# Optimization experiments

Measured on AMD Instinct MI355X. Metric: run time of the kernel, lower is better.

Reference implementation:

```python
import jax, jax.numpy as jnp
import numpy as np

DIM = 768
N_HEADS = 12
HEAD_DIM = DIM // N_HEADS
B, T = 2, 2048


def setup_inputs() -> dict:
    key = jax.random.key(0)
    ks = jax.random.split(key, 11)
    s = 0.02
    return {
        "q_in": jax.random.normal(ks[0], (B, T, DIM), jnp.float32),
        "k_in": jax.random.normal(ks[1], (B, T, DIM), jnp.float32),
        "v_in": jax.random.normal(ks[2], (B, T, DIM), jnp.float32),
        "Wq": jax.random.normal(ks[3], (DIM, DIM), jnp.float32) * s,
        "bq": jnp.zeros((DIM,), jnp.float32),
        "Wk": jax.random.normal(ks[4], (DIM, DIM), jnp.float32) * s,
        "bk": jnp.zeros((DIM,), jnp.float32),
        "Wv": jax.random.normal(ks[5], (DIM, DIM), jnp.float32) * s,
        "bv": jnp.zeros((DIM,), jnp.float32),
        "Wo": jax.random.normal(ks[6], (DIM, DIM), jnp.float32) * s,
        "bo": jnp.zeros((DIM,), jnp.float32),
    }


def reference(q_in, k_in, v_in, Wq, bq, Wk, bk, Wv, bv, Wo, bo):
    b, t, c = q_in.shape
    scale = HEAD_DIM ** -0.5
    # linear projections (torch Linear: x @ W.T + b)
    q = q_in @ Wq.T + bq
    k = k_in @ Wk.T + bk
    v = v_in @ Wv.T + bv
    # [b, t, h, d] -> [b, h, t, d]
    q = q.reshape(b, t, N_HEADS, HEAD_DIM).transpose(0, 2, 1, 3)
    k = k.reshape(b, t, N_HEADS, HEAD_DIM).transpose(0, 2, 1, 3)
    v = v.reshape(b, t, N_HEADS, HEAD_DIM).transpose(0, 2, 1, 3)
    scores = jnp.einsum("bhqd,bhkd->bhqk", q, k) * scale  # full TxT scores
    probs = jax.nn.softmax(scores, axis=-1)
    attn = jnp.einsum("bhqk,bhkd->bhqd", probs, v)
    attn = attn.transpose(0, 2, 1, 3).reshape(b, t, c)
    return attn @ Wo.T + bo
```

## Files before the change

kernel.cpp:

```cpp
#include <hip/hip_runtime.h>


typedef unsigned short u16;
typedef __attribute__((ext_vector_type(8))) short short8;
typedef __attribute__((ext_vector_type(4))) short short4v;
typedef __attribute__((ext_vector_type(4))) float float4v;

#define DIMC 768
#define NTOK 4096
#define NHD  12
#define HDD  64
#define SEQT 2048

#if __has_builtin(__builtin_amdgcn_mfma_f32_16x16x16bf16_1k)
#define HAVE_MFMA16 1
#else
#define HAVE_MFMA16 0
#endif

__device__ __forceinline__ u16 f2bf(float f) {
  union { float f; unsigned u; } v; v.f = f;
  unsigned r = v.u + 0x7fffu + ((v.u >> 16) & 1u);
  return (u16)(r >> 16);
}
__device__ __forceinline__ float bf2f(u16 u) {
  union { unsigned u; float f; } v; v.u = ((unsigned)u) << 16;
  return v.f;
}
__device__ __forceinline__ short4v u2s4(uint2 u) {
  union { uint2 u; short4v s; } v; v.u = u; return v.s;
}

__global__ __launch_bounds__(256) void cvt_all(
    const float* __restrict__ a0, const float* __restrict__ a1, const float* __restrict__ a2,
    const float* __restrict__ a3, const float* __restrict__ a4, const float* __restrict__ a5,
    const float* __restrict__ a6,
    u16* __restrict__ o0, u16* __restrict__ o1, u16* __restrict__ o2,
    u16* __restrict__ o3, u16* __restrict__ o4, u16* __restrict__ o5,
    u16* __restrict__ o6) {
  int bid = blockIdx.x;
  const float* s; u16* d; int inner;
  if (bid < 9216) {
    int z = bid / 3072; inner = bid - z * 3072;
    s = (z == 0) ? a0 : (z == 1) ? a1 : a2;
    d = (z == 0) ? o0 : (z == 1) ? o1 : o2;
  } else {
    int r = bid - 9216; int z = r / 576; inner = r - z * 576;
    s = (z == 0) ? a3 : (z == 1) ? a4 : (z == 2) ? a5 : a6;
    d = (z == 0) ? o3 : (z == 1) ? o4 : (z == 2) ? o5 : o6;
  }
  size_t i = ((size_t)inner * 256 + threadIdx.x) * 4;
  float4 v = *(const float4*)(s + i);
  *(ushort4*)(d + i) = make_ushort4(f2bf(v.x), f2bf(v.y), f2bf(v.z), f2bf(v.w));
}

__device__ __forceinline__ void gemm_mainloop3(
    const u16* __restrict__ X, const u16* __restrict__ W,
    int m0, int n0, u16* Als, u16* Bls, float4v acc[4][4]) {
  int tid = threadIdx.x;
  int sr = tid >> 3, sc = (tid & 7) * 8;
  int w = tid >> 6, lane = tid & 63, quad = lane >> 4, r15 = lane & 15;
  int wm = (w >> 1) * 64, wn = (w & 1) * 64;
  const u16* xp0 = X + (size_t)(m0 + sr) * DIMC + sc;
  const u16* xp1 = xp0 + 32 * DIMC;
  const u16* xp2 = xp0 + 64 * DIMC;
  const u16* xp3 = xp0 + 96 * DIMC;
  const u16* wp0 = W + (size_t)(n0 + sr) * DIMC + sc;
  const u16* wp1 = wp0 + 32 * DIMC;
  const u16* wp2 = wp0 + 64 * DIMC;
  const u16* wp3 = wp0 + 96 * DIMC;
  uint4 pa0 = *(const uint4*)xp0, pa1 = *(const uint4*)xp1;
  uint4 pa2 = *(const uint4*)xp2, pa3 = *(const uint4*)xp3;
  uint4 pb0 = *(const uint4*)wp0, pb1 = *(const uint4*)wp1;
  uint4 pb2 = *(const uint4*)wp2, pb3 = *(const uint4*)wp3;
  for (int k0 = 0; k0 < DIMC; k0 += 64) {
    __syncthreads();
    *(uint4*)(Als + sr * 72 + sc) = pa0;
    *(uint4*)(Als + (sr + 32) * 72 + sc) = pa1;
    *(uint4*)(Als + (sr + 64) * 72 + sc) = pa2;
    *(uint4*)(Als + (sr + 96) * 72 + sc) = pa3;
    *(uint4*)(Bls + sr * 72 + sc) = pb0;
    *(uint4*)(Bls + (sr + 32) * 72 + sc) = pb1;
    *(uint4*)(Bls + (sr + 64) * 72 + sc) = pb2;
    *(uint4*)(Bls + (sr + 96) * 72 + sc) = pb3;
    __syncthreads();
    int kn = k0 + 64;
    if (kn < DIMC) {
      pa0 = *(const uint4*)(xp0 + kn); pa1 = *(const uint4*)(xp1 + kn);
      pa2 = *(const uint4*)(xp2 + kn); pa3 = *(const uint4*)(xp3 + kn);
      pb0 = *(const uint4*)(wp0 + kn); pb1 = *(const uint4*)(wp1 + kn);
      pb2 = *(const uint4*)(wp2 + kn); pb3 = *(const uint4*)(wp3 + kn);
    }
    #pragma unroll
    for (int sk = 0; sk < 2; sk++) {
      short8 af[4], bf[4];
      #pragma unroll
      for (int mf = 0; mf < 4; mf++)
        af[mf] = *(const short8*)(Als + (wm + mf * 16 + r15) * 72 + sk * 32 + quad * 8);
      #pragma unroll
      for (int nf = 0; nf < 4; nf++)
        bf[nf] = *(const short8*)(Bls + (wn + nf * 16 + r15) * 72 + sk * 32 + quad * 8);
      #pragma unroll
      for (int mf = 0; mf < 4; mf++)
        #pragma unroll
        for (int nf = 0; nf < 4; nf++)
          acc[mf][nf] = __builtin_amdgcn_mfma_f32_16x16x32_bf16(af[mf], bf[nf], acc[mf][nf], 0, 0, 0);
    }
  }
}

__global__ __launch_bounds__(256, 2) void gemm_qkv(
    const u16* __restrict__ xq, const u16* __restrict__ xk, const u16* __restrict__ xv,
    const u16* __restrict__ wq, const u16* __restrict__ wk, const u16* __restrict__ wv,
    const float* __restrict__ bq, const float* __restrict__ bk, const float* __restrict__ bv,
    u16* __restrict__ Qh, u16* __restrict__ Kh, u16* __restrict__ Vt) {
  __shared__ __align__(16) u16 LS[2 * 128 * 72];
  u16* Als = LS;
  u16* Bls = LS + 128 * 72;
  int z = blockIdx.z;
  const u16* X = (z == 0) ? xq : (z == 1) ? xk : xv;
  const u16* W = (z == 0) ? wq : (z == 1) ? wk : wv;
  const float* bias = (z == 0) ? bq : (z == 1) ? bk : bv;
  int m0 = blockIdx.x * 128, n0 = blockIdx.y * 128;
  float4v acc[4][4];
  #pragma unroll
  for (int i = 0; i < 4; i++)
    #pragma unroll
    for (int j = 0; j < 4; j++)
      #pragma unroll
      for (int r = 0; r < 4; r++) acc[i][j][r] = 0.f;
  gemm_mainloop3(X, W, m0, n0, Als, Bls, acc);
  int tid = threadIdx.x, w = tid >> 6, lane = tid & 63, quad = lane >> 4, r15 = lane & 15;
  int wm = (w >> 1) * 64, wn = (w & 1) * 64;
  if (z == 2) {
    __syncthreads();
    u16* T = LS;
    #pragma unroll
    for (int mf = 0; mf < 4; mf++)
      #pragma unroll
      for (int nf = 0; nf < 4; nf++)
        #pragma unroll
        for (int rg = 0; rg < 4; rg++) {
          int mloc = wm + mf * 16 + quad * 4 + rg;
          int nloc = wn + nf * 16 + r15;
          T[nloc * 136 + mloc] = f2bf(acc[mf][nf][rg] + bias[n0 + nloc]);
        }
    __syncthreads();
    int r = tid >> 1, seg = tid & 1;
    int b = m0 >> 11, t0 = m0 & 2047;
    int h = (n0 + r) >> 6, d = (n0 + r) & 63;
    size_t base = (((size_t)(b * NHD + h)) * HDD + d) * SEQT + t0 + seg * 64;
    const u16* src = T + r * 136 + seg * 64;
    #pragma unroll
    for (int j = 0; j < 8; j++)
      *(uint4*)(Vt + base + j * 8) = *(const uint4*)(src + j * 8);
  } else {
    #pragma unroll
    for (int mf = 0; mf < 4; mf++)
      #pragma unroll
      for (int nf = 0; nf < 4; nf++)
        #pragma unroll
        for (int rg = 0; rg < 4; rg++) {
          int m = m0 + wm + mf * 16 + quad * 4 + rg;
          int n = n0 + wn + nf * 16 + r15;
          float val = acc[mf][nf][rg] + bias[n];
          if (z == 0) val *= 0.180336880f;
          int b = m >> 11, t = m & 2047, h = n >> 6, d = n & 63;
          u16 o = f2bf(val);
          size_t bh = (size_t)(b * NHD + h);
          if (z == 0) Qh[(bh * SEQT + t) * HDD + d] = o;
          else Kh[(bh * SEQT + t) * HDD + d] = o;
        }
  }
}

__global__ __launch_bounds__(256, 4) void attn_kernel(
    const u16* __restrict__ Qh, const u16* __restrict__ Kh, const u16* __restrict__ Vt,
    u16* __restrict__ Opart, float* __restrict__ Lpart) {
  __shared__ __align__(16) u16 Kls[64 * 64];
  __shared__ __align__(16) u16 Vls[64 * 64];
#if !HAVE_MFMA16
  __shared__ __align__(16) u16 Pls[4 * 32 * 64];
#endif
  int bh = blockIdx.y, sp = blockIdx.z, qt0 = blockIdx.x * 128;
  int tid = threadIdx.x, w = tid >> 6, lane = tid & 63, quad = lane >> 4, r15 = lane & 15;
  int qw = qt0 + w * 32;
  const int nt = 8;
  int kt0 = sp * (nt * 64);

  int rr = r15 & 7;
  int sx0 = (quad ^ rr) * 8;
  int sx1 = ((4 + quad) ^ rr) * 8;
  int q1 = quad >> 1, q0 = quad & 1;

  short8 qa[2][2];
  #pragma unroll
  for (int qs = 0; qs < 2; qs++) {
    const u16* qp = Qh + ((size_t)bh * SEQT + qw + qs * 16 + r15) * HDD + quad * 8;
    qa[qs][0] = *(const short8*)qp;
    qa[qs][1] = *(const short8*)(qp + 32);
  }
  float4v fzero;
  #pragma unroll
  for (int r = 0; r < 4; r++) fzero[r] = 0.f;

  float4v oacc[2][4];
  float lsum[2];
  #pragma unroll
  for (int qs = 0; qs < 2; qs++) {
    lsum[qs] = 0.f;
    #pragma unroll
    for (int dt = 0; dt < 4; dt++)
      #pragma unroll
      for (int r = 0; r < 4; r++) oacc[qs][dt][r] = 0.f;
  }

  const u16* Kbase = Kh + (size_t)bh * SEQT * HDD;
  const u16* Vbase = Vt + (size_t)bh * HDD * SEQT;
  int sr = tid >> 3, sc = (tid & 7) * 8;
  int sg = (((tid & 7) ^ (sr & 7)) * 8);

  uint4 pk0 = *(const uint4*)(Kbase + (size_t)(kt0 + sr) * HDD + sc);
  uint4 pk1 = *(const uint4*)(Kbase + (size_t)(kt0 + sr + 32) * HDD + sc);
  uint4 pv0 = *(const uint4*)(Vbase + (size_t)sr * SEQT + kt0 + sc);
  uint4 pv1 = *(const uint4*)(Vbase + (size_t)(sr + 32) * SEQT + kt0 + sc);

  for (int it = 0; it < nt; it++) {
    __syncthreads();
    *(uint4*)(Kls + sr * 64 + sg) = pk0;
    *(uint4*)(Kls + (sr + 32) * 64 + sg) = pk1;
    *(uint4*)(Vls + sr * 64 + sg) = pv0;
    *(uint4*)(Vls + (sr + 32) * 64 + sg) = pv1;
    __syncthreads();
    int nit = it + 1; if (nit == nt) nit = 0;
    int ktn = kt0 + nit * 64;
    pk0 = *(const uint4*)(Kbase + (size_t)(ktn + sr) * HDD + sc);
    pk1 = *(const uint4*)(Kbase + (size_t)(ktn + sr + 32) * HDD + sc);
    pv0 = *(const uint4*)(Vbase + (size_t)sr * SEQT + ktn + sc);
    pv1 = *(const uint4*)(Vbase + (size_t)(sr + 32) * SEQT + ktn + sc);

    __builtin_amdgcn_s_setprio(1);
#if HAVE_MFMA16
    #pragma unroll
    for (int nk = 0; nk < 4; nk++) {
      short8 k0 = *(const short8*)(Kls + (nk * 16 + r15) * 64 + sx0);
      short8 k1 = *(const short8*)(Kls + (nk * 16 + r15) * 64 + sx1);
      float4v z0 = __builtin_amdgcn_mfma_f32_16x16x32_bf16(k0, qa[0][0], fzero, 0, 0, 0);
      z0 = __builtin_amdgcn_mfma_f32_16x16x32_bf16(k1, qa[0][1], z0, 0, 0, 0);
      float4v z1 = __builtin_amdgcn_mfma_f32_16x16x32_bf16(k0, qa[1][0], fzero, 0, 0, 0);
      z1 = __builtin_amdgcn_mfma_f32_16x16x32_bf16(k1, qa[1][1], z1, 0, 0, 0);
      float a0 = __builtin_amdgcn_exp2f(z0[0]);
      float a1 = __builtin_amdgcn_exp2f(z0[1]);
      float a2 = __builtin_amdgcn_exp2f(z0[2]);
      float a3 = __builtin_amdgcn_exp2f(z0[3]);
      float b0 = __builtin_amdgcn_exp2f(z1[0]);
      float b1 = __builtin_amdgcn_exp2f(z1[1]);
      float b2 = __builtin_amdgcn_exp2f(z1[2]);
      float b3 = __builtin_amdgcn_exp2f(z1[3]);
      lsum[0] += (a0 + a1) + (a2 + a3);
      lsum[1] += (b0 + b1) + (b2 + b3);
      short4v pb0 = u2s4(make_uint2(
          __builtin_amdgcn_perm(__float_as_uint(a1), __float_as_uint(a0), 0x07060302u),
          __builtin_amdgcn_perm(__float_as_uint(a3), __float_as_uint(a2), 0x07060302u)));
      short4v pb1 = u2s4(make_uint2(
          __builtin_amdgcn_perm(__float_as_uint(b1), __float_as_uint(b0), 0x07060302u),
          __builtin_amdgcn_perm(__float_as_uint(b3), __float_as_uint(b2), 0x07060302u)));
      #pragma unroll
      for (int dt = 0; dt < 4; dt++) {
        uint2 vw = *(const uint2*)(Vls + (dt * 16 + r15) * 64 +
                                   (((nk * 2 + q1) ^ rr) * 8) + q0 * 4);
        short4v va = u2s4(vw);
        oacc[0][dt] = __builtin_amdgcn_mfma_f32_16x16x16bf16_1k(va, pb0, oacc[0][dt], 0, 0, 0);
        oacc[1][dt] = __builtin_amdgcn_mfma_f32_16x16x16bf16_1k(va, pb1, oacc[1][dt], 0, 0, 0);
      }
    }
#else
    u16* Pw = Pls + w * (32 * 64);
    #pragma unroll
    for (int nk = 0; nk < 4; nk++) {
      short8 k0 = *(const short8*)(Kls + (nk * 16 + r15) * 64 + sx0);
      short8 k1 = *(const short8*)(Kls + (nk * 16 + r15) * 64 + sx1);
      #pragma unroll
      for (int qs = 0; qs < 2; qs++) {
        float4v zv = __builtin_amdgcn_mfma_f32_16x16x32_bf16(k0, qa[qs][0], fzero, 0, 0, 0);
        zv = __builtin_amdgcn_mfma_f32_16x16x32_bf16(k1, qa[qs][1], zv, 0, 0, 0);
        float p0 = __builtin_amdgcn_exp2f(zv[0]);
        float p1 = __builtin_amdgcn_exp2f(zv[1]);
        float p2 = __builtin_amdgcn_exp2f(zv[2]);
        float p3 = __builtin_amdgcn_exp2f(zv[3]);
        lsum[qs] += (p0 + p1) + (p2 + p3);
        unsigned lo = __builtin_amdgcn_perm(__float_as_uint(p1), __float_as_uint(p0), 0x07060302u);
        unsigned hi = __builtin_amdgcn_perm(__float_as_uint(p3), __float_as_uint(p2), 0x07060302u);
        *(uint2*)(Pw + (qs * 16 + r15) * 64 + (((nk * 4 + quad) ^ (rr << 1)) << 2)) =
            make_uint2(lo, hi);
      }
    }
    short8 pa[2][2];
    #pragma unroll
    for (int qs = 0; qs < 2; qs++) {
      pa[qs][0] = *(const short8*)(Pw + (qs * 16 + r15) * 64 + sx0);
      pa[qs][1] = *(const short8*)(Pw + (qs * 16 + r15) * 64 + sx1);
    }
    #pragma unroll
    for (int dt = 0; dt < 4; dt++) {
      short8 v0 = *(const short8*)(Vls + (dt * 16 + r15) * 64 + sx0);
      short8 v1 = *(const short8*)(Vls + (dt * 16 + r15) * 64 + sx1);
      #pragma unroll
      for (int qs = 0; qs < 2; qs++) {
        oacc[qs][dt] = __builtin_amdgcn_mfma_f32_16x16x32_bf16(pa[qs][0], v0, oacc[qs][dt], 0, 0, 0);
        oacc[qs][dt] = __builtin_amdgcn_mfma_f32_16x16x32_bf16(pa[qs][1], v1, oacc[qs][dt], 0, 0, 0);
      }
    }
#endif
    __builtin_amdgcn_s_setprio(0);
  }
  size_t obase = ((size_t)sp * 2 * NHD + bh) * SEQT + qw;
#if HAVE_MFMA16
  #pragma unroll
  for (int qs = 0; qs < 2; qs++) {
    u16* orow = Opart + (obase + qs * 16 + r15) * HDD + quad * 4;
    #pragma unroll
    for (int dt = 0; dt < 4; dt++) {
      u16 c0 = f2bf(oacc[qs][dt][0]);
      u16 c1 = f2bf(oacc[qs][dt][1]);
      u16 c2 = f2bf(oacc[qs][dt][2]);
      u16 c3 = f2bf(oacc[qs][dt][3]);
      *(uint2*)(orow + dt * 16) =
          make_uint2((unsigned)c0 | ((unsigned)c1 << 16),
                     (unsigned)c2 | ((unsigned)c3 << 16));
    }
  }
#else
  #pragma unroll
  for (int qs = 0; qs < 2; qs++)
    #pragma unroll
    for (int rg = 0; rg < 4; rg++) {
      u16* orow = Opart + (obase + qs * 16 + quad * 4 + rg) * HDD;
      #pragma unroll
      for (int dt = 0; dt < 4; dt++) orow[dt * 16 + r15] = f2bf(oacc[qs][dt][rg]);
    }
#endif
  #pragma unroll
  for (int qs = 0; qs < 2; qs++) {
    float s = lsum[qs];
    s += __shfl_xor(s, 16, 64);
    s += __shfl_xor(s, 32, 64);
    if (quad == 0) Lpart[obase + qs * 16 + r15] = s;
  }
}

__global__ __launch_bounds__(256) void merge_kernel(
    const u16* __restrict__ Opart, const float* __restrict__ Lpart, u16* __restrict__ X2) {
  const size_t NXe = (size_t)2 * NHD * SEQT * HDD;
  const size_t LS = (size_t)2 * NHD * SEQT;
  int tid = threadIdx.x;
  int row = blockIdx.x * 32 + (tid >> 3);
  int dcol = (tid & 7) * 8;
  int bh = row >> 11, t = row & 2047;
  size_t off = (size_t)row * HDD + dcol;
  float inv = 1.0f / (Lpart[row] + Lpart[row + LS] +
                      Lpart[row + 2 * LS] + Lpart[row + 3 * LS]);
  int b = bh / NHD, h = bh % NHD;
  u16 o[8];
  #pragma unroll
  for (int half = 0; half < 2; half++) {
    ushort4 a = *(const ushort4*)(Opart + off + half * 4);
    ushort4 c = *(const ushort4*)(Opart + off + NXe + half * 4);
    ushort4 e = *(const ushort4*)(Opart + off + 2 * NXe + half * 4);
    ushort4 g = *(const ushort4*)(Opart + off + 3 * NXe + half * 4);
    o[half * 4 + 0] = f2bf((bf2f(a.x) + bf2f(c.x) + bf2f(e.x) + bf2f(g.x)) * inv);
    o[half * 4 + 1] = f2bf((bf2f(a.y) + bf2f(c.y) + bf2f(e.y) + bf2f(g.y)) * inv);
    o[half * 4 + 2] = f2bf((bf2f(a.z) + bf2f(c.z) + bf2f(e.z) + bf2f(g.z)) * inv);
    o[half * 4 + 3] = f2bf((bf2f(a.w) + bf2f(c.w) + bf2f(e.w) + bf2f(g.w)) * inv);
  }
  *(uint4*)(X2 + ((size_t)b * SEQT + t) * DIMC + h * HDD + dcol) = *(uint4*)o;
}

__global__ __launch_bounds__(256, 2) void gemm_out(
    const u16* __restrict__ X2, const u16* __restrict__ wo,
    const float* __restrict__ bo, float* __restrict__ out) {
  __shared__ __align__(16) u16 LS[2 * 128 * 72];
  u16* Als = LS;
  u16* Bls = LS + 128 * 72;
  int m0 = blockIdx.x * 128, n0 = blockIdx.y * 128;
  float4v acc[4][4];
  #pragma unroll
  for (int i = 0; i < 4; i++)
    #pragma unroll
    for (int j = 0; j < 4; j++)
      #pragma unroll
      for (int r = 0; r < 4; r++) acc[i][j][r] = 0.f;
  gemm_mainloop3(X2, wo, m0, n0, Als, Bls, acc);
  int tid = threadIdx.x, w = tid >> 6, lane = tid & 63, quad = lane >> 4, r15 = lane & 15;
  int wm = (w >> 1) * 64, wn = (w & 1) * 64;
  #pragma unroll
  for (int mf = 0; mf < 4; mf++)
    #pragma unroll
    for (int nf = 0; nf < 4; nf++)
      #pragma unroll
      for (int rg = 0; rg < 4; rg++) {
        int m = m0 + wm + mf * 16 + quad * 4 + rg;
        int n = n0 + wn + nf * 16 + r15;
        out[(size_t)m * DIMC + n] = acc[mf][nf][rg] + bo[n];
      }
}

extern "C" void kernel_launch(void* const* d_in, const int* in_sizes, int n_in,
                              void* d_out, int out_size, void* d_ws, size_t ws_size,
                              hipStream_t stream) {
  const float* q_in = (const float*)d_in[0];
  const float* k_in = (const float*)d_in[1];
  const float* v_in = (const float*)d_in[2];
  const float* Wq = (const float*)d_in[3];
  const float* bq = (const float*)d_in[4];
  const float* Wk = (const float*)d_in[5];
  const float* bk = (const float*)d_in[6];
  const float* Wv = (const float*)d_in[7];
  const float* bv = (const float*)d_in[8];
  const float* Wo = (const float*)d_in[9];
  const float* bo = (const float*)d_in[10];

  const size_t NX = (size_t)NTOK * DIMC;
  const size_t NW = (size_t)DIMC * DIMC;
  u16* ws = (u16*)d_ws;
  u16* qb = ws;
  u16* kb = qb + NX;
  u16* vb = kb + NX;
  u16* wqb = vb + NX;
  u16* wkb = wqb + NW;
  u16* wvb = wkb + NW;
  u16* wob = wvb + NW;
  u16* Qh = wob + NW;
  u16* Kh = Qh + NX;
  u16* Vt = Kh + NX;
  u16* X2 = Vt + NX;
  u16* Opart = X2 + NX;
  float* Lpart = (float*)(Opart + 4 * NX);

  cvt_all<<<dim3(11520), 256, 0, stream>>>(
      q_in, k_in, v_in, Wq, Wk, Wv, Wo, qb, kb, vb, wqb, wkb, wvb, wob);
  gemm_qkv<<<dim3(NTOK / 128, DIMC / 128, 3), 256, 0, stream>>>(
      qb, kb, vb, wqb, wkb, wvb, bq, bk, bv, Qh, Kh, Vt);
  attn_kernel<<<dim3(SEQT / 128, 2 * NHD, 4), 256, 0, stream>>>(Qh, Kh, Vt, Opart, Lpart);
  merge_kernel<<<dim3(2 * NHD * SEQT / 32), 256, 0, stream>>>(Opart, Lpart, X2);
  gemm_out<<<dim3(NTOK / 128, DIMC / 128), 256, 0, stream>>>(X2, wob, bo, (float*)d_out);
}
```

Before: 184.9 us.

## Double-buffer K/V tiles in LDS and swizzle V halves to cut bank conflicts

The attention kernel moves from a single LDS K/V buffer, which needed two barriers per tile, to ping-pong buffers. This leaves one barrier per tile, and the next tile is staged while the current one is computed. V tile halves are also swapped on store according to row bit 3, and the read offset is adjusted to match, to reduce LDS bank conflicts on the 8-byte V reads. The non-MFMA16 fallback path is removed. LDS use doubles to 32KB per block, which could reduce occupancy under the launch bound of 4 blocks.

```diff
diff --git a/kernel.cpp b/kernel.cpp
--- a/kernel.cpp
+++ b/kernel.cpp
@@ -11,12 +11,6 @@
 #define NHD  12
 #define HDD  64
 #define SEQT 2048
-
-#if __has_builtin(__builtin_amdgcn_mfma_f32_16x16x16bf16_1k)
-#define HAVE_MFMA16 1
-#else
-#define HAVE_MFMA16 0
-#endif
 
 __device__ __forceinline__ u16 f2bf(float f) {
   union { float f; unsigned u; } v; v.f = f;
@@ -177,21 +171,20 @@
 __global__ __launch_bounds__(256, 4) void attn_kernel(
     const u16* __restrict__ Qh, const u16* __restrict__ Kh, const u16* __restrict__ Vt,
     u16* __restrict__ Opart, float* __restrict__ Lpart) {
-  __shared__ __align__(16) u16 Kls[64 * 64];
-  __shared__ __align__(16) u16 Vls[64 * 64];
-#if !HAVE_MFMA16
-  __shared__ __align__(16) u16 Pls[4 * 32 * 64];
-#endif
+  __shared__ __align__(16) u16 K0ls[64 * 64];
+  __shared__ __align__(16) u16 V0ls[64 * 64];
+  __shared__ __align__(16) u16 K1ls[64 * 64];
+  __shared__ __align__(16) u16 V1ls[64 * 64];
   int bh = blockIdx.y, sp = blockIdx.z, qt0 = blockIdx.x * 128;
   int tid = threadIdx.x, w = tid >> 6, lane = tid & 63, quad = lane >> 4, r15 = lane & 15;
   int qw = qt0 + w * 32;
-  const int nt = 8;
-  int kt0 = sp * (nt * 64);
+  int kt0 = sp * 512;
 
   int rr = r15 & 7;
   int sx0 = (quad ^ rr) * 8;
   int sx1 = ((4 + quad) ^ rr) * 8;
   int q1 = quad >> 1, q0 = quad & 1;
+  int q0h = (q0 ^ (r15 >> 3)) * 4;
 
   short8 qa[2][2];
   #pragma unroll
@@ -219,32 +212,29 @@
   const u16* Vbase = Vt + (size_t)bh * HDD * SEQT;
   int sr = tid >> 3, sc = (tid & 7) * 8;
   int sg = (((tid & 7) ^ (sr & 7)) * 8);
-
-  uint4 pk0 = *(const uint4*)(Kbase + (size_t)(kt0 + sr) * HDD + sc);
-  uint4 pk1 = *(const uint4*)(Kbase + (size_t)(kt0 + sr + 32) * HDD + sc);
-  uint4 pv0 = *(const uint4*)(Vbase + (size_t)sr * SEQT + kt0 + sc);
-  uint4 pv1 = *(const uint4*)(Vbase + (size_t)(sr + 32) * SEQT + kt0 + sc);
-
-  for (int it = 0; it < nt; it++) {
-    __syncthreads();
-    *(uint4*)(Kls + sr * 64 + sg) = pk0;
-    *(uint4*)(Kls + (sr + 32) * 64 + sg) = pk1;
-    *(uint4*)(Vls + sr * 64 + sg) = pv0;
-    *(uint4*)(Vls + (sr + 32) * 64 + sg) = pv1;
-    __syncthreads();
-    int nit = it + 1; if (nit == nt) nit = 0;
-    int ktn = kt0 + nit * 64;
-    pk0 = *(const uint4*)(Kbase + (size_t)(ktn + sr) * HDD + sc);
-    pk1 = *(const uint4*)(Kbase + (size_t)(ktn + sr + 32) * HDD + sc);
-    pv0 = *(const uint4*)(Vbase + (size_t)sr * SEQT + ktn + sc);
-    pv1 = *(const uint4*)(Vbase + (size_t)(sr + 32) * SEQT + ktn + sc);
-
+  int hs = (sr >> 3) & 1;
+
+  uint4 pk0, pk1, pv0, pv1;
+  auto load_tile = [&](int kt) {
+    pk0 = *(const uint4*)(Kbase + (size_t)(kt + sr) * HDD + sc);
+    pk1 = *(const uint4*)(Kbase + (size_t)(kt + sr + 32) * HDD + sc);
+    pv0 = *(const uint4*)(Vbase + (size_t)sr * SEQT + kt + sc);
+    pv1 = *(const uint4*)(Vbase + (size_t)(sr + 32) * SEQT + kt + sc);
+  };
+  auto stage_tile = [&](u16* Kd, u16* Vd) {
+    *(uint4*)(Kd + sr * 64 + sg) = pk0;
+    *(uint4*)(Kd + (sr + 32) * 64 + sg) = pk1;
+    uint4 w0 = hs ? make_uint4(pv0.z, pv0.w, pv0.x, pv0.y) : pv0;
+    uint4 w1 = hs ? make_uint4(pv1.z, pv1.w, pv1.x, pv1.y) : pv1;
+    *(uint4*)(Vd + sr * 64 + sg) = w0;
+    *(uint4*)(Vd + (sr + 32) * 64 + sg) = w1;
+  };
+  auto compute_tile = [&](const u16* Kc, const u16* Vc) {
     __builtin_amdgcn_s_setprio(1);
-#if HAVE_MFMA16
     #pragma unroll
     for (int nk = 0; nk < 4; nk++) {
-      short8 k0 = *(const short8*)(Kls + (nk * 16 + r15) * 64 + sx0);
-      short8 k1 = *(const short8*)(Kls + (nk * 16 + r15) * 64 + sx1);
+      short8 k0 = *(const short8*)(Kc + (nk * 16 + r15) * 64 + sx0);
+      short8 k1 = *(const short8*)(Kc + (nk * 16 + r15) * 64 + sx1);
       float4v z0 = __builtin_amdgcn_mfma_f32_16x16x32_bf16(k0, qa[0][0], fzero, 0, 0, 0);
       z0 = __builtin_amdgcn_mfma_f32_16x16x32_bf16(k1, qa[0][1], z0, 0, 0, 0);
       float4v z1 = __builtin_amdgcn_mfma_f32_16x16x32_bf16(k0, qa[1][0], fzero, 0, 0, 0);
@@ -267,55 +257,36 @@
           __builtin_amdgcn_perm(__float_as_uint(b3), __float_as_uint(b2), 0x07060302u)));
       #pragma unroll
       for (int dt = 0; dt < 4; dt++) {
-        uint2 vw = *(const uint2*)(Vls + (dt * 16 + r15) * 64 +
-                                   (((nk * 2 + q1) ^ rr) * 8) + q0 * 4);
+        uint2 vw = *(const uint2*)(Vc + (dt * 16 + r15) * 64 +
+                                   (((nk * 2 + q1) ^ rr) * 8) + q0h);
         short4v va = u2s4(vw);
         oacc[0][dt] = __builtin_amdgcn_mfma_f32_16x16x16bf16_1k(va, pb0, oacc[0][dt], 0, 0, 0);
         oacc[1][dt] = __builtin_amdgcn_mfma_f32_16x16x16bf16_1k(va, pb1, oacc[1][dt], 0, 0, 0);
       }
     }
-#else
-    u16* Pw = Pls + w * (32 * 64);
-    #pragma unroll
-    for (int nk = 0; nk < 4; nk++) {
-      short8 k0 = *(const short8*)(Kls + (nk * 16 + r15) * 64 + sx0);
-      short8 k1 = *(const short8*)(Kls + (nk * 16 + r15) * 64 + sx1);
-      #pragma unroll
-      for (int qs = 0; qs < 2; qs++) {
-        float4v zv = __builtin_amdgcn_mfma_f32_16x16x32_bf16(k0, qa[qs][0], fzero, 0, 0, 0);
-        zv = __builtin_amdgcn_mfma_f32_16x16x32_bf16(k1, qa[qs][1], zv, 0, 0, 0);
-        float p0 = __builtin_amdgcn_exp2f(zv[0]);
-        float p1 = __builtin_amdgcn_exp2f(zv[1]);
-        float p2 = __builtin_amdgcn_exp2f(zv[2]);
-        float p3 = __builtin_amdgcn_exp2f(zv[3]);
-        lsum[qs] += (p0 + p1) + (p2 + p3);
-        unsigned lo = __builtin_amdgcn_perm(__float_as_uint(p1), __float_as_uint(p0), 0x07060302u);
-        unsigned hi = __builtin_amdgcn_perm(__float_as_uint(p3), __float_as_uint(p2), 0x07060302u);
-        *(uint2*)(Pw + (qs * 16 + r15) * 64 + (((nk * 4 + quad) ^ (rr << 1)) << 2)) =
-            make_uint2(lo, hi);
-      }
+    __builtin_amdgcn_s_setprio(0);
+  };
+
+  load_tile(kt0);
+  stage_tile(K0ls, V0ls);
+  __syncthreads();
+  #pragma unroll
+  for (int ib = 0; ib < 4; ib++) {
+    load_tile(kt0 + (ib * 2 + 1) * 64);
+    compute_tile(K0ls, V0ls);
+    stage_tile(K1ls, V1ls);
+    __syncthreads();
+    if (ib < 3) {
+      load_tile(kt0 + (ib * 2 + 2) * 64);
+      compute_tile(K1ls, V1ls);
+      stage_tile(K0ls, V0ls);
+      __syncthreads();
+    } else {
+      compute_tile(K1ls, V1ls);
     }
-    short8 pa[2][2];
-    #pragma unroll
-    for (int qs = 0; qs < 2; qs++) {
-      pa[qs][0] = *(const short8*)(Pw + (qs * 16 + r15) * 64 + sx0);
-      pa[qs][1] = *(const short8*)(Pw + (qs * 16 + r15) * 64 + sx1);
-    }
-    #pragma unroll
-    for (int dt = 0; dt < 4; dt++) {
-      short8 v0 = *(const short8*)(Vls + (dt * 16 + r15) * 64 + sx0);
-      short8 v1 = *(const short8*)(Vls + (dt * 16 + r15) * 64 + sx1);
-      #pragma unroll
-      for (int qs = 0; qs < 2; qs++) {
-        oacc[qs][dt] = __builtin_amdgcn_mfma_f32_16x16x32_bf16(pa[qs][0], v0, oacc[qs][dt], 0, 0, 0);
-        oacc[qs][dt] = __builtin_amdgcn_mfma_f32_16x16x32_bf16(pa[qs][1], v1, oacc[qs][dt], 0, 0, 0);
-      }
-    }
-#endif
-    __builtin_amdgcn_s_setprio(0);
-  }
+  }
+
   size_t obase = ((size_t)sp * 2 * NHD + bh) * SEQT + qw;
-#if HAVE_MFMA16
   #pragma unroll
   for (int qs = 0; qs < 2; qs++) {
     u16* orow = Opart + (obase + qs * 16 + r15) * HDD + quad * 4;
@@ -330,16 +301,6 @@
                      (unsigned)c2 | ((unsigned)c3 << 16));
     }
   }
-#else
-  #pragma unroll
-  for (int qs = 0; qs < 2; qs++)
-    #pragma unroll
-    for (int rg = 0; rg < 4; rg++) {
-      u16* orow = Opart + (obase + qs * 16 + quad * 4 + rg) * HDD;
-      #pragma unroll
-      for (int dt = 0; dt < 4; dt++) orow[dt * 16 + r15] = f2bf(oacc[qs][dt][rg]);
-    }
-#endif
   #pragma unroll
   for (int qs = 0; qs < 2; qs++) {
     float s = lsum[qs];
```

Measured after the change: 316.2 us. 71.1% more time.
